# Kernel optimization log

Measured on AMD Instinct MI355X. Metric: run time of the kernel, lower is better.

Reference implementation:

```python
import jax, jax.numpy as jnp
import numpy as np

EMBED = 768
HEADS = 12
HEAD_DIM = EMBED // HEADS
B, T = 2, 2048


def setup_inputs() -> dict:
    key = jax.random.key(0)
    ks = jax.random.split(key, 5)
    scale = 0.02
    return {
        "x": jax.random.normal(ks[0], (B, T, EMBED), dtype=jnp.float32),
        "Wq": jax.random.normal(ks[1], (HEADS, EMBED, HEAD_DIM), dtype=jnp.float32) * scale,
        "Wk": jax.random.normal(ks[2], (HEADS, EMBED, HEAD_DIM), dtype=jnp.float32) * scale,
        "Wv": jax.random.normal(ks[3], (HEADS, EMBED, HEAD_DIM), dtype=jnp.float32) * scale,
        "Wp": jax.random.normal(ks[4], (EMBED, EMBED), dtype=jnp.float32) * scale,
        "bp": jnp.zeros((EMBED,), dtype=jnp.float32),
    }


def reference(x, Wq, Wk, Wv, Wp, bp):
    # x: [B,T,E]; per-head projections batched over the head axis.
    q = jnp.einsum("bte,hed->bhtd", x, Wq)  # [B,H,T,Dh]
    k = jnp.einsum("bte,hed->bhtd", x, Wk)
    v = jnp.einsum("bte,hed->bhtd", x, Wv)
    scale = 1.0 / jnp.sqrt(jnp.asarray(HEAD_DIM, dtype=x.dtype))
    scores = jnp.einsum("bhtd,bhsd->bhts", q, k) * scale  # [B,H,T,T]
    Tlen = x.shape[1]
    causal = jnp.tril(jnp.ones((Tlen, Tlen), dtype=bool))
    scores = jnp.where(causal[None, None], scores, jnp.asarray(-jnp.inf, dtype=scores.dtype))
    attn = jax.nn.softmax(scores, axis=-1)
    out = jnp.einsum("bhts,bhsd->bhtd", attn, v)  # [B,H,T,Dh]
    # concat heads (same layout as torch.cat over per-head outputs)
    out = out.transpose(0, 2, 1, 3).reshape(x.shape[0], Tlen, HEADS * HEAD_DIM)
    return out @ Wp + bp
```

## Files before the change

### kernel.cpp

```cpp
#include <hip/hip_runtime.h>
#include <math.h>

namespace {

constexpr int E_  = 768;
constexpr int H_  = 12;
constexpr int DH_ = 64;
constexpr int T_  = 2048;
constexpr int B_  = 2;
constexpr int M_  = B_ * T_;
constexpr int BH_ = B_ * H_;

typedef __attribute__((ext_vector_type(8))) short bf16x8;
typedef __attribute__((ext_vector_type(4))) float f32x4;

__device__ inline ushort f2bf(float f) {
  union { float f; unsigned u; } v; v.f = f;
  unsigned u = v.u + 0x7FFFu + ((v.u >> 16) & 1u);
  return (ushort)(u >> 16);
}
__device__ inline float bf2f(ushort u) {
  union { unsigned u; float f; } v; v.u = (unsigned)u << 16; return v.f;
}

__device__ __forceinline__ void gl16(const ushort* g, ushort* l) {
  __builtin_amdgcn_global_load_lds(
      (const __attribute__((address_space(1))) unsigned int*)(g),
      (__attribute__((address_space(3))) unsigned int*)(l), 16, 0, 0);
}

constexpr int NCONV = 1536;

__global__ __launch_bounds__(256) void prep_k(
    const float* __restrict__ x,
    const float* __restrict__ Wq, const float* __restrict__ Wk,
    const float* __restrict__ Wv, const float* __restrict__ Wp,
    ushort* __restrict__ xb, ushort* __restrict__ Wt, ushort* __restrict__ Wpt)
{
  __shared__ float tile[64][65];
  const int bid = blockIdx.x;
  const int tid = threadIdx.x;

  if (bid < NCONV) {
    const size_t i = ((size_t)bid * 256 + tid) * 8;
    float4 a = *(const float4*)(x + i);
    float4 b = *(const float4*)(x + i + 4);
    ushort o[8] = {f2bf(a.x), f2bf(a.y), f2bf(a.z), f2bf(a.w),
                   f2bf(b.x), f2bf(b.y), f2bf(b.z), f2bf(b.w)};
    *(bf16x8*)(xb + i) = *(bf16x8*)o;
    return;
  }

  const int wb = bid - NCONV;
  const int tr = tid >> 4, tc = tid & 15;
  const float* src; ushort* dst;
  int k0, n0, sN, dK;
  if (wb < 432) {
    const int mat = wb / 144, rem = wb % 144;
    const int h = rem / 12, ktile = rem % 12;
    const float* W = (mat == 0) ? Wq : (mat == 1) ? Wk : Wv;
    src = W + (size_t)h * E_ * DH_;
    dst = Wt + (size_t)(mat * H_ + h) * DH_ * E_;
    k0 = ktile * 64; n0 = 0; sN = DH_; dK = E_;
  } else {
    const int rem = wb - 432;
    src = Wp;
    dst = Wpt;
    k0 = (rem / 12) * 64; n0 = (rem % 12) * 64; sN = E_; dK = E_;
  }

#pragma unroll
  for (int rr = 0; rr < 64; rr += 16) {
    float4 v = *(const float4*)(src + (size_t)(k0 + tr + rr) * sN + n0 + tc * 4);
    tile[tr + rr][tc * 4 + 0] = v.x;
    tile[tr + rr][tc * 4 + 1] = v.y;
    tile[tr + rr][tc * 4 + 2] = v.z;
    tile[tr + rr][tc * 4 + 3] = v.w;
  }
  __syncthreads();
#pragma unroll
  for (int rr = 0; rr < 64; rr += 16) {
    const int n = tr + rr;
    ushort4 o;
    o.x = f2bf(tile[tc * 4 + 0][n]);
    o.y = f2bf(tile[tc * 4 + 1][n]);
    o.z = f2bf(tile[tc * 4 + 2][n]);
    o.w = f2bf(tile[tc * 4 + 3][n]);
    *(ushort4*)(dst + (size_t)(n0 + n) * dK + k0 + tc * 4) = o;
  }
}

constexpr float QSCALE = 0.18033688f;

__global__ __launch_bounds__(256) void qkv_fused_k(
    const ushort* __restrict__ xb, const ushort* __restrict__ Wt,
    ushort* __restrict__ q_ws, ushort* __restrict__ k_ws, ushort* __restrict__ vt_ws)
{
  __shared__ __align__(16) ushort lds[2 * 128 * 64];
  ushort* As = lds;
  ushort* Bs = lds + 128 * 64;

  const int n0 = blockIdx.x * 128;
  const int m0 = blockIdx.y * 128;

  const int tid  = threadIdx.x;
  const int w    = tid >> 6, l = tid & 63;
  const int lrow = l & 15, lk = l >> 4;
  const int r7   = lrow & 7;
  const int srow = l >> 3;
  const int sch  = (l & 7) ^ srow;

  f32x4 acc[2][8] = {};

  for (int k0 = 0; k0 < E_; k0 += 64) {
#pragma unroll
    for (int r = 0; r < 4; ++r) {
      const int base = r * 32 + w * 8;
      gl16(xb + (size_t)(m0 + base + srow) * E_ + k0 + sch * 8, &As[base * 64]);
      gl16(Wt + (size_t)(n0 + base + srow) * E_ + k0 + sch * 8, &Bs[base * 64]);
    }
    __syncthreads();

#pragma unroll
    for (int kk = 0; kk < 2; ++kk) {
      const int cof = ((kk * 4 + lk) ^ r7) * 8;
      const bf16x8 a0 = *(const bf16x8*)&As[(w * 32 + lrow) * 64 + cof];
      const bf16x8 a1 = *(const bf16x8*)&As[(w * 32 + 16 + lrow) * 64 + cof];
#pragma unroll
      for (int nf = 0; nf < 8; ++nf) {
        const bf16x8 b = *(const bf16x8*)&Bs[(nf * 16 + lrow) * 64 + cof];
        acc[0][nf] = __builtin_amdgcn_mfma_f32_16x16x32_bf16(a0, b, acc[0][nf], 0, 0, 0);
        acc[1][nf] = __builtin_amdgcn_mfma_f32_16x16x32_bf16(a1, b, acc[1][nf], 0, 0, 0);
      }
    }
    __syncthreads();
  }

  const int b  = m0 >> 11;
  const int t0 = m0 & 2047;
  ushort* Td = lds;

#pragma unroll
  for (int half = 0; half < 2; ++half) {
    const int seg = (n0 >> 6) + half;
    const int mat = seg / H_;
    const int h   = seg - mat * H_;
    const int bh  = b * H_ + h;

    if (mat != 2) {
      const float qs = (mat == 0) ? QSCALE : 1.0f;
      ushort* outw = (mat == 0) ? q_ws : k_ws;
#pragma unroll
      for (int mi = 0; mi < 2; ++mi)
#pragma unroll
        for (int i = 0; i < 4; ++i) {
          const int t = t0 + w * 32 + mi * 16 + lk * 4 + i;
          ushort* orow = outw + ((size_t)bh * T_ + t) * DH_;
#pragma unroll
          for (int nf2 = 0; nf2 < 4; ++nf2)
            orow[nf2 * 16 + lrow] = f2bf(acc[mi][half * 4 + nf2][i] * qs);
        }
    } else {
      __syncthreads();
#pragma unroll
      for (int mi = 0; mi < 2; ++mi)
#pragma unroll
        for (int i = 0; i < 4; ++i) {
          const int tl = w * 32 + mi * 16 + lk * 4 + i;
#pragma unroll
          for (int nf2 = 0; nf2 < 4; ++nf2)
            Td[(nf2 * 16 + lrow) * 136 + tl] = f2bf(acc[mi][half * 4 + nf2][i]);
        }
      __syncthreads();
#pragma unroll
      for (int it = 0; it < 4; ++it) {
        const int c = tid + it * 256;
        const int d = c >> 4, sub = c & 15;
        *(bf16x8*)(vt_ws + ((size_t)bh * DH_ + d) * T_ + t0 + sub * 8) =
            *(const bf16x8*)&Td[d * 136 + sub * 8];
      }
    }
  }
}

__global__ __launch_bounds__(256) void attn_split_k(
    const ushort* __restrict__ q_ws, const ushort* __restrict__ k_ws,
    const ushort* __restrict__ vt_ws, ushort* __restrict__ op_ws,
    float2* __restrict__ ml_ws)
{
  __shared__ __align__(16) ushort Ks[64 * 64];
  __shared__ __align__(16) ushort Vt[64 * 64];
  __shared__ __align__(16) ushort Pl[4][16 * 64];

  const int qt = 31 - (int)blockIdx.y;
  const int bh = blockIdx.x;
  const int hz = blockIdx.z;
  const int nt = qt + 1;
  const int klo = hz ? (nt >> 1) : 0;
  const int khi = hz ? nt : (nt >> 1);
  const int q0 = qt * 64;

  const ushort* Qb  = q_ws + (size_t)bh * T_ * DH_;
  const ushort* Kb  = k_ws + (size_t)bh * T_ * DH_;
  const ushort* VTb = vt_ws + (size_t)bh * DH_ * T_;

  const int tid  = threadIdx.x;
  const int w    = tid >> 6;
  const int l    = tid & 63;
  const int lrow = l & 15;
  const int lk   = l >> 4;
  const int r7   = lrow & 7;
  const int rr   = tid >> 3;
  const int sub  = tid & 7;
  const int swc  = sub ^ (rr & 7);

  const int st0 = rr * 64 + swc * 8;
  const int st1 = (rr + 32) * 64 + swc * 8;

  int kof0[4], kof1[4];
#pragma unroll
  for (int ct = 0; ct < 4; ++ct) {
    kof0[ct] = (ct * 16 + lrow) * 64 + ((lk ^ r7) * 8);
    kof1[ct] = (ct * 16 + lrow) * 64 + (((lk + 4) ^ r7) * 8);
  }

  const ushort* Qrow = Qb + (size_t)(q0 + w * 16 + lrow) * DH_;
  const bf16x8 qa0 = *(const bf16x8*)(Qrow + lk * 8);
  const bf16x8 qa1 = *(const bf16x8*)(Qrow + lk * 8 + 32);
  const int qglob = q0 + w * 16 + lrow;

  float m_r = -INFINITY, l_r = 0.f;
  f32x4 oc[4] = {};

  ushort* Pw = &Pl[w][0];
  const int rd0 = lrow * 64 + ((lk ^ r7) * 8);
  const int rd1 = lrow * 64 + (((lk + 4) ^ r7) * 8);
  const int wrbase  = lrow * 128 + (lk & 1) * 8;
  const int wrchunk = (lk >> 1);

  if (klo < khi) {
    bf16x8 kp0 = *(const bf16x8*)(Kb + (size_t)(klo * 64 + rr) * DH_ + sub * 8);
    bf16x8 kp1 = *(const bf16x8*)(Kb + (size_t)(klo * 64 + rr + 32) * DH_ + sub * 8);
    bf16x8 vp0 = *(const bf16x8*)(VTb + (size_t)rr * T_ + klo * 64 + sub * 8);
    bf16x8 vp1 = *(const bf16x8*)(VTb + (size_t)(rr + 32) * T_ + klo * 64 + sub * 8);

    for (int kt = klo; kt < khi; ++kt) {
      const int s0 = kt * 64;

      *(bf16x8*)&Ks[st0] = kp0;
      *(bf16x8*)&Ks[st1] = kp1;
      *(bf16x8*)&Vt[st0] = vp0;
      *(bf16x8*)&Vt[st1] = vp1;
      __syncthreads();

      if (kt + 1 < khi) {
        const int sn = s0 + 64;
        kp0 = *(const bf16x8*)(Kb + (size_t)(sn + rr) * DH_ + sub * 8);
        kp1 = *(const bf16x8*)(Kb + (size_t)(sn + rr + 32) * DH_ + sub * 8);
        vp0 = *(const bf16x8*)(VTb + (size_t)rr * T_ + sn + sub * 8);
        vp1 = *(const bf16x8*)(VTb + (size_t)(rr + 32) * T_ + sn + sub * 8);
      }

      f32x4 st[4];
#pragma unroll
      for (int ct = 0; ct < 4; ++ct) {
        const bf16x8 kb0 = *(const bf16x8*)&Ks[kof0[ct]];
        const bf16x8 kb1 = *(const bf16x8*)&Ks[kof1[ct]];
        f32x4 z = {0.f, 0.f, 0.f, 0.f};
        z = __builtin_amdgcn_mfma_f32_16x16x32_bf16(kb0, qa0, z, 0, 0, 0);
        st[ct] = __builtin_amdgcn_mfma_f32_16x16x32_bf16(kb1, qa1, z, 0, 0, 0);
      }

      if (kt == qt) {
#pragma unroll
        for (int ct = 0; ct < 4; ++ct)
#pragma unroll
          for (int i = 0; i < 4; ++i)
            if (s0 + ct * 16 + lk * 4 + i > qglob) st[ct][i] = -INFINITY;
      }

      float mc[4];
#pragma unroll
      for (int ct = 0; ct < 4; ++ct)
        mc[ct] = fmaxf(fmaxf(st[ct][0], st[ct][1]), fmaxf(st[ct][2], st[ct][3]));
      float mx = fmaxf(fmaxf(mc[0], mc[1]), fmaxf(mc[2], mc[3]));
      mx = fmaxf(mx, __shfl_xor(mx, 16));
      mx = fmaxf(mx, __shfl_xor(mx, 32));

      if (__any(mx > m_r + 8.f)) {
        const float mn   = fmaxf(m_r, mx);
        const float corr = exp2f(m_r - mn);
        m_r = mn;
        l_r *= corr;
#pragma unroll
        for (int i = 0; i < 4; ++i) {
          const float cr = __shfl(corr, lk * 4 + i);
#pragma unroll
          for (int ct = 0; ct < 4; ++ct) oc[ct][i] *= cr;
        }
      }

      float sc[4];
#pragma unroll
      for (int ct = 0; ct < 4; ++ct) {
#pragma unroll
        for (int i = 0; i < 4; ++i) st[ct][i] = exp2f(st[ct][i] - m_r);
        sc[ct] = (st[ct][0] + st[ct][1]) + (st[ct][2] + st[ct][3]);
      }
      float rs = (sc[0] + sc[1]) + (sc[2] + sc[3]);
      rs += __shfl_xor(rs, 16);
      rs += __shfl_xor(rs, 32);
      l_r += rs;

#pragma unroll
      for (int ct = 0; ct < 4; ++ct) {
        unsigned lo, hi;
        asm("v_cvt_pk_bf16_f32 %0, %1, %2" : "=v"(lo) : "v"(st[ct][0]), "v"(st[ct][1]));
        asm("v_cvt_pk_bf16_f32 %0, %1, %2" : "=v"(hi) : "v"(st[ct][2]), "v"(st[ct][3]));
        uint2 pk; pk.x = lo; pk.y = hi;
        const int ch = ((ct * 2 + wrchunk) ^ r7);
        *(uint2*)((char*)Pw + wrbase + ch * 16) = pk;
      }

      const bf16x8 pa0 = *(const bf16x8*)(Pw + rd0);
      const bf16x8 pa1 = *(const bf16x8*)(Pw + rd1);

#pragma unroll
      for (int ct = 0; ct < 4; ++ct) {
        const bf16x8 vb0 = *(const bf16x8*)&Vt[kof0[ct]];
        const bf16x8 vb1 = *(const bf16x8*)&Vt[kof1[ct]];
        oc[ct] = __builtin_amdgcn_mfma_f32_16x16x32_bf16(pa0, vb0, oc[ct], 0, 0, 0);
        oc[ct] = __builtin_amdgcn_mfma_f32_16x16x32_bf16(pa1, vb1, oc[ct], 0, 0, 0);
      }
      __syncthreads();
    }
  }

  const size_t pb = (size_t)(hz * BH_ + bh) * T_;
  if (lk == 0)
    ml_ws[pb + q0 + w * 16 + lrow] = make_float2(m_r, l_r);
#pragma unroll
  for (int i = 0; i < 4; ++i) {
    const int t = q0 + w * 16 + lk * 4 + i;
    ushort* orow = op_ws + (pb + t) * DH_;
#pragma unroll
    for (int ct = 0; ct < 4; ++ct)
      orow[ct * 16 + lrow] = f2bf(oc[ct][i]);
  }
}

__global__ __launch_bounds__(256) void attn_combine_k(
    const ushort* __restrict__ op_ws, const float2* __restrict__ ml_ws,
    ushort* __restrict__ o_ws)
{
  const int bh = blockIdx.x;
  const int t  = blockIdx.y * 64 + (threadIdx.x >> 2);
  const int d0 = (threadIdx.x & 3) * 16;

  const size_t ixA = (size_t)bh * T_ + t;
  const size_t ixB = (size_t)(BH_ + bh) * T_ + t;
  const float2 mlA = ml_ws[ixA];
  const float2 mlB = ml_ws[ixB];
  const float m   = fmaxf(mlA.x, mlB.x);
  const float wA  = exp2f(mlA.x - m);
  const float wB  = exp2f(mlB.x - m);
  const float inv = 1.0f / (wA * mlA.y + wB * mlB.y);

  const ushort* pA = op_ws + ixA * DH_ + d0;
  const ushort* pB = op_ws + ixB * DH_ + d0;
  bf16x8 a0 = *(const bf16x8*)pA;
  bf16x8 a1 = *(const bf16x8*)(pA + 8);
  bf16x8 b0 = *(const bf16x8*)pB;
  bf16x8 b1 = *(const bf16x8*)(pB + 8);

  ushort o[16];
#pragma unroll
  for (int j = 0; j < 8; ++j) {
    o[j]     = f2bf((wA * bf2f((ushort)a0[j]) + wB * bf2f((ushort)b0[j])) * inv);
    o[8 + j] = f2bf((wA * bf2f((ushort)a1[j]) + wB * bf2f((ushort)b1[j])) * inv);
  }
  const int bb = bh / H_, hh = bh - (bh / H_) * H_;
  ushort* po = o_ws + ((size_t)bb * T_ + t) * E_ + hh * DH_ + d0;
  *(bf16x8*)po       = *(const bf16x8*)&o[0];
  *(bf16x8*)(po + 8) = *(const bf16x8*)&o[8];
}

__global__ __launch_bounds__(256) void proj2_k(
    const ushort* __restrict__ ob, const ushort* __restrict__ Wpt,
    const float* __restrict__ bp, float* __restrict__ out)
{
  __shared__ __align__(16) ushort lds[2 * 128 * 64];
  ushort* As = lds;
  ushort* Bs = lds + 128 * 64;

  const int n0 = blockIdx.x * 128;
  const int m0 = blockIdx.y * 128;

  const int tid  = threadIdx.x;
  const int w    = tid >> 6, l = tid & 63;
  const int lrow = l & 15, lk = l >> 4;
  const int r7   = lrow & 7;
  const int srow = l >> 3;
  const int sch  = (l & 7) ^ srow;

  f32x4 acc[2][8] = {};

  for (int k0 = 0; k0 < E_; k0 += 64) {
#pragma unroll
    for (int r = 0; r < 4; ++r) {
      const int base = r * 32 + w * 8;
      gl16(ob  + (size_t)(m0 + base + srow) * E_ + k0 + sch * 8, &As[base * 64]);
      gl16(Wpt + (size_t)(n0 + base + srow) * E_ + k0 + sch * 8, &Bs[base * 64]);
    }
    __syncthreads();

#pragma unroll
    for (int kk = 0; kk < 2; ++kk) {
      const int cof = ((kk * 4 + lk) ^ r7) * 8;
      const bf16x8 a0 = *(const bf16x8*)&As[(w * 32 + lrow) * 64 + cof];
      const bf16x8 a1 = *(const bf16x8*)&As[(w * 32 + 16 + lrow) * 64 + cof];
#pragma unroll
      for (int nf = 0; nf < 8; ++nf) {
        const bf16x8 b = *(const bf16x8*)&Bs[(nf * 16 + lrow) * 64 + cof];
        acc[0][nf] = __builtin_amdgcn_mfma_f32_16x16x32_bf16(a0, b, acc[0][nf], 0, 0, 0);
        acc[1][nf] = __builtin_amdgcn_mfma_f32_16x16x32_bf16(a1, b, acc[1][nf], 0, 0, 0);
      }
    }
    __syncthreads();
  }

  float bias[8];
#pragma unroll
  for (int nf = 0; nf < 8; ++nf) bias[nf] = bp[n0 + nf * 16 + lrow];

#pragma unroll
  for (int mi = 0; mi < 2; ++mi)
#pragma unroll
    for (int i = 0; i < 4; ++i) {
      const int m = m0 + w * 32 + mi * 16 + lk * 4 + i;
      float* orow = out + (size_t)m * E_ + n0;
#pragma unroll
      for (int nf = 0; nf < 8; ++nf)
        orow[nf * 16 + lrow] = acc[mi][nf][i] + bias[nf];
    }
}

}

extern "C" void kernel_launch(void* const* d_in, const int* in_sizes, int n_in,
                              void* d_out, int out_size, void* d_ws, size_t ws_size,
                              hipStream_t stream) {
  const float* x  = (const float*)d_in[0];
  const float* Wq = (const float*)d_in[1];
  const float* Wk = (const float*)d_in[2];
  const float* Wv = (const float*)d_in[3];
  const float* Wp = (const float*)d_in[4];
  const float* bp = (const float*)d_in[5];
  float* out = (float*)d_out;

  const size_t nx  = (size_t)M_ * E_;
  const size_t nwt = (size_t)3 * H_ * DH_ * E_;
  const size_t nwp = (size_t)E_ * E_;
  const size_t per = (size_t)BH_ * T_ * DH_;

  ushort* xb    = (ushort*)d_ws;
  ushort* Wt    = xb + nx;
  ushort* Wpt   = Wt + nwt;
  ushort* q_ws  = Wpt + nwp;
  ushort* k_ws  = q_ws + per;
  ushort* vt_ws = k_ws + per;
  ushort* o_b   = vt_ws + per;
  ushort* op_ws = o_b + per;
  float2* ml_ws = (float2*)(op_ws + 2 * per);

  prep_k<<<dim3(NCONV + 576), 256, 0, stream>>>(x, Wq, Wk, Wv, Wp, xb, Wt, Wpt);
  qkv_fused_k<<<dim3(18, 32), 256, 0, stream>>>(xb, Wt, q_ws, k_ws, vt_ws);
  attn_split_k<<<dim3(24, 32, 2), 256, 0, stream>>>(q_ws, k_ws, vt_ws, op_ws, ml_ws);
  attn_combine_k<<<dim3(24, 32), 256, 0, stream>>>(op_ws, ml_ws, o_b);
  proj2_k<<<dim3(6, 32), 256, 0, stream>>>(o_b, Wpt, bp, out);
}
```

Before: 102.3 us.

## Fuse split-attention combine into projection GEMM and shrink QKV tile width

```diff
diff --git a/kernel.cpp b/kernel.cpp
--- a/kernel.cpp
+++ b/kernel.cpp
@@ -96,12 +96,14 @@
     const ushort* __restrict__ xb, const ushort* __restrict__ Wt,
     ushort* __restrict__ q_ws, ushort* __restrict__ k_ws, ushort* __restrict__ vt_ws)
 {
-  __shared__ __align__(16) ushort lds[2 * 128 * 64];
+  __shared__ __align__(16) ushort lds[(128 + 64) * 64];
   ushort* As = lds;
   ushort* Bs = lds + 128 * 64;
 
-  const int n0 = blockIdx.x * 128;
-  const int m0 = blockIdx.y * 128;
+  const int seg = blockIdx.x;
+  const int n0g = 0;
+  const int m0  = blockIdx.y * 128;
+  const ushort* Wh = Wt + (size_t)seg * DH_ * E_;
 
   const int tid  = threadIdx.x;
   const int w    = tid >> 6, l = tid & 63;
@@ -110,14 +112,15 @@
   const int srow = l >> 3;
   const int sch  = (l & 7) ^ srow;
 
-  f32x4 acc[2][8] = {};
+  f32x4 acc[2][4] = {};
 
   for (int k0 = 0; k0 < E_; k0 += 64) {
 #pragma unroll
     for (int r = 0; r < 4; ++r) {
       const int base = r * 32 + w * 8;
       gl16(xb + (size_t)(m0 + base + srow) * E_ + k0 + sch * 8, &As[base * 64]);
-      gl16(Wt + (size_t)(n0 + base + srow) * E_ + k0 + sch * 8, &Bs[base * 64]);
+      if (r < 2)
+        gl16(Wh + (size_t)(n0g + base + srow) * E_ + k0 + sch * 8, &Bs[base * 64]);
     }
     __syncthreads();
 
@@ -127,7 +130,7 @@
       const bf16x8 a0 = *(const bf16x8*)&As[(w * 32 + lrow) * 64 + cof];
       const bf16x8 a1 = *(const bf16x8*)&As[(w * 32 + 16 + lrow) * 64 + cof];
 #pragma unroll
-      for (int nf = 0; nf < 8; ++nf) {
+      for (int nf = 0; nf < 4; ++nf) {
         const bf16x8 b = *(const bf16x8*)&Bs[(nf * 16 + lrow) * 64 + cof];
         acc[0][nf] = __builtin_amdgcn_mfma_f32_16x16x32_bf16(a0, b, acc[0][nf], 0, 0, 0);
         acc[1][nf] = __builtin_amdgcn_mfma_f32_16x16x32_bf16(a1, b, acc[1][nf], 0, 0, 0);
@@ -136,49 +139,44 @@
     __syncthreads();
   }
 
-  const int b  = m0 >> 11;
-  const int t0 = m0 & 2047;
-  ushort* Td = lds;
-
-#pragma unroll
-  for (int half = 0; half < 2; ++half) {
-    const int seg = (n0 >> 6) + half;
-    const int mat = seg / H_;
-    const int h   = seg - mat * H_;
-    const int bh  = b * H_ + h;
-
-    if (mat != 2) {
-      const float qs = (mat == 0) ? QSCALE : 1.0f;
-      ushort* outw = (mat == 0) ? q_ws : k_ws;
-#pragma unroll
-      for (int mi = 0; mi < 2; ++mi)
-#pragma unroll
-        for (int i = 0; i < 4; ++i) {
-          const int t = t0 + w * 32 + mi * 16 + lk * 4 + i;
-          ushort* orow = outw + ((size_t)bh * T_ + t) * DH_;
-#pragma unroll
-          for (int nf2 = 0; nf2 < 4; ++nf2)
-            orow[nf2 * 16 + lrow] = f2bf(acc[mi][half * 4 + nf2][i] * qs);
-        }
-    } else {
-      __syncthreads();
-#pragma unroll
-      for (int mi = 0; mi < 2; ++mi)
-#pragma unroll
-        for (int i = 0; i < 4; ++i) {
-          const int tl = w * 32 + mi * 16 + lk * 4 + i;
-#pragma unroll
-          for (int nf2 = 0; nf2 < 4; ++nf2)
-            Td[(nf2 * 16 + lrow) * 136 + tl] = f2bf(acc[mi][half * 4 + nf2][i]);
-        }
-      __syncthreads();
-#pragma unroll
-      for (int it = 0; it < 4; ++it) {
-        const int c = tid + it * 256;
-        const int d = c >> 4, sub = c & 15;
-        *(bf16x8*)(vt_ws + ((size_t)bh * DH_ + d) * T_ + t0 + sub * 8) =
-            *(const bf16x8*)&Td[d * 136 + sub * 8];
-      }
+  const int b   = m0 >> 11;
+  const int t0  = m0 & 2047;
+  const int mat = seg / H_;
+  const int h   = seg - mat * H_;
+  const int bh  = b * H_ + h;
+
+  if (mat != 2) {
+    const float qs = (mat == 0) ? QSCALE : 1.0f;
+    ushort* outw = (mat == 0) ? q_ws : k_ws;
+#pragma unroll
+    for (int mi = 0; mi < 2; ++mi)
+#pragma unroll
+      for (int i = 0; i < 4; ++i) {
+        const int t = t0 + w * 32 + mi * 16 + lk * 4 + i;
+        ushort* orow = outw + ((size_t)bh * T_ + t) * DH_;
+#pragma unroll
+        for (int nf = 0; nf < 4; ++nf)
+          orow[nf * 16 + lrow] = f2bf(acc[mi][nf][i] * qs);
+      }
+  } else {
+    ushort* Td = lds;
+    __syncthreads();
+#pragma unroll
+    for (int mi = 0; mi < 2; ++mi)
+#pragma unroll
+      for (int i = 0; i < 4; ++i) {
+        const int tl = w * 32 + mi * 16 + lk * 4 + i;
+#pragma unroll
+        for (int nf = 0; nf < 4; ++nf)
+          Td[(nf * 16 + lrow) * 136 + tl] = f2bf(acc[mi][nf][i]);
+      }
+    __syncthreads();
+#pragma unroll
+    for (int it = 0; it < 4; ++it) {
+      const int c = tid + it * 256;
+      const int d = c >> 4, sub = c & 15;
+      *(bf16x8*)(vt_ws + ((size_t)bh * DH_ + d) * T_ + t0 + sub * 8) =
+          *(const bf16x8*)&Td[d * 136 + sub * 8];
     }
   }
 }
@@ -349,52 +347,19 @@
   }
 }
 
-__global__ __launch_bounds__(256) void attn_combine_k(
+__global__ __launch_bounds__(256) void proj_fused_k(
     const ushort* __restrict__ op_ws, const float2* __restrict__ ml_ws,
-    ushort* __restrict__ o_ws)
+    const ushort* __restrict__ Wpt, const float* __restrict__ bp,
+    float* __restrict__ out)
 {
-  const int bh = blockIdx.x;
-  const int t  = blockIdx.y * 64 + (threadIdx.x >> 2);
-  const int d0 = (threadIdx.x & 3) * 16;
-
-  const size_t ixA = (size_t)bh * T_ + t;
-  const size_t ixB = (size_t)(BH_ + bh) * T_ + t;
-  const float2 mlA = ml_ws[ixA];
-  const float2 mlB = ml_ws[ixB];
-  const float m   = fmaxf(mlA.x, mlB.x);
-  const float wA  = exp2f(mlA.x - m);
-  const float wB  = exp2f(mlB.x - m);
-  const float inv = 1.0f / (wA * mlA.y + wB * mlB.y);
-
-  const ushort* pA = op_ws + ixA * DH_ + d0;
-  const ushort* pB = op_ws + ixB * DH_ + d0;
-  bf16x8 a0 = *(const bf16x8*)pA;
-  bf16x8 a1 = *(const bf16x8*)(pA + 8);
-  bf16x8 b0 = *(const bf16x8*)pB;
-  bf16x8 b1 = *(const bf16x8*)(pB + 8);
-
-  ushort o[16];
-#pragma unroll
-  for (int j = 0; j < 8; ++j) {
-    o[j]     = f2bf((wA * bf2f((ushort)a0[j]) + wB * bf2f((ushort)b0[j])) * inv);
-    o[8 + j] = f2bf((wA * bf2f((ushort)a1[j]) + wB * bf2f((ushort)b1[j])) * inv);
-  }
-  const int bb = bh / H_, hh = bh - (bh / H_) * H_;
-  ushort* po = o_ws + ((size_t)bb * T_ + t) * E_ + hh * DH_ + d0;
-  *(bf16x8*)po       = *(const bf16x8*)&o[0];
-  *(bf16x8*)(po + 8) = *(const bf16x8*)&o[8];
-}
-
-__global__ __launch_bounds__(256) void proj2_k(
-    const ushort* __restrict__ ob, const ushort* __restrict__ Wpt,
-    const float* __restrict__ bp, float* __restrict__ out)
-{
-  __shared__ __align__(16) ushort lds[2 * 128 * 64];
+  __shared__ __align__(16) ushort lds[(64 + 64) * 64];
   ushort* As = lds;
-  ushort* Bs = lds + 128 * 64;
-
-  const int n0 = blockIdx.x * 128;
-  const int m0 = blockIdx.y * 128;
+  ushort* Bs = lds + 64 * 64;
+
+  const int n0 = blockIdx.x * 64;
+  const int m0 = blockIdx.y * 64;
+  const int b  = m0 >> 11;
+  const int t0 = m0 & 2047;
 
   const int tid  = threadIdx.x;
   const int w    = tid >> 6, l = tid & 63;
@@ -402,47 +367,76 @@
   const int r7   = lrow & 7;
   const int srow = l >> 3;
   const int sch  = (l & 7) ^ srow;
-
-  f32x4 acc[2][8] = {};
+  const int ar = tid >> 2;
+  const int cc = tid & 3;
+  const int a7 = ar & 7;
+
+  f32x4 acc[4] = {};
 
   for (int k0 = 0; k0 < E_; k0 += 64) {
-#pragma unroll
-    for (int r = 0; r < 4; ++r) {
+    const int h  = k0 >> 6;
+    const int bh = b * H_ + h;
+
+#pragma unroll
+    for (int r = 0; r < 2; ++r) {
       const int base = r * 32 + w * 8;
-      gl16(ob  + (size_t)(m0 + base + srow) * E_ + k0 + sch * 8, &As[base * 64]);
       gl16(Wpt + (size_t)(n0 + base + srow) * E_ + k0 + sch * 8, &Bs[base * 64]);
+    }
+
+    {
+      const int t = t0 + ar;
+      const size_t ixA = (size_t)bh * T_ + t;
+      const size_t ixB = (size_t)(BH_ + bh) * T_ + t;
+      const float2 mlA = ml_ws[ixA];
+      const float2 mlB = ml_ws[ixB];
+      const float m   = fmaxf(mlA.x, mlB.x);
+      const float wA  = exp2f(mlA.x - m);
+      const float wB  = exp2f(mlB.x - m);
+      const float inv = 1.0f / (wA * mlA.y + wB * mlB.y);
+      const float fA = wA * inv, fB = wB * inv;
+
+      const ushort* pA = op_ws + ixA * DH_ + cc * 16;
+      const ushort* pB = op_ws + ixB * DH_ + cc * 16;
+      bf16x8 a0 = *(const bf16x8*)pA;
+      bf16x8 a1 = *(const bf16x8*)(pA + 8);
+      bf16x8 b0 = *(const bf16x8*)pB;
+      bf16x8 b1 = *(const bf16x8*)(pB + 8);
+      ushort o[16];
+#pragma unroll
+      for (int j = 0; j < 8; ++j) {
+        o[j]     = f2bf(fA * bf2f((ushort)a0[j]) + fB * bf2f((ushort)b0[j]));
+        o[8 + j] = f2bf(fA * bf2f((ushort)a1[j]) + fB * bf2f((ushort)b1[j]));
+      }
+      *(bf16x8*)&As[ar * 64 + ((2 * cc) ^ a7) * 8]     = *(const bf16x8*)&o[0];
+      *(bf16x8*)&As[ar * 64 + ((2 * cc + 1) ^ a7) * 8] = *(const bf16x8*)&o[8];
     }
     __syncthreads();
 
 #pragma unroll
     for (int kk = 0; kk < 2; ++kk) {
       const int cof = ((kk * 4 + lk) ^ r7) * 8;
-      const bf16x8 a0 = *(const bf16x8*)&As[(w * 32 + lrow) * 64 + cof];
-      const bf16x8 a1 = *(const bf16x8*)&As[(w * 32 + 16 + lrow) * 64 + cof];
-#pragma unroll
-      for (int nf = 0; nf < 8; ++nf) {
-        const bf16x8 b = *(const bf16x8*)&Bs[(nf * 16 + lrow) * 64 + cof];
-        acc[0][nf] = __builtin_amdgcn_mfma_f32_16x16x32_bf16(a0, b, acc[0][nf], 0, 0, 0);
-        acc[1][nf] = __builtin_amdgcn_mfma_f32_16x16x32_bf16(a1, b, acc[1][nf], 0, 0, 0);
-      }
-    }
-    __syncthreads();
-  }
-
-  float bias[8];
-#pragma unroll
-  for (int nf = 0; nf < 8; ++nf) bias[nf] = bp[n0 + nf * 16 + lrow];
-
-#pragma unroll
-  for (int mi = 0; mi < 2; ++mi)
-#pragma unroll
-    for (int i = 0; i < 4; ++i) {
-      const int m = m0 + w * 32 + mi * 16 + lk * 4 + i;
-      float* orow = out + (size_t)m * E_ + n0;
-#pragma unroll
-      for (int nf = 0; nf < 8; ++nf)
-        orow[nf * 16 + lrow] = acc[mi][nf][i] + bias[nf];
-    }
+      const bf16x8 a = *(const bf16x8*)&As[(w * 16 + lrow) * 64 + cof];
+#pragma unroll
+      for (int nf = 0; nf < 4; ++nf) {
+        const bf16x8 bb = *(const bf16x8*)&Bs[(nf * 16 + lrow) * 64 + cof];
+        acc[nf] = __builtin_amdgcn_mfma_f32_16x16x32_bf16(a, bb, acc[nf], 0, 0, 0);
+      }
+    }
+    __syncthreads();
+  }
+
+  float bias[4];
+#pragma unroll
+  for (int nf = 0; nf < 4; ++nf) bias[nf] = bp[n0 + nf * 16 + lrow];
+
+#pragma unroll
+  for (int i = 0; i < 4; ++i) {
+    const int m = m0 + w * 16 + lk * 4 + i;
+    float* orow = out + (size_t)m * E_ + n0;
+#pragma unroll
+    for (int nf = 0; nf < 4; ++nf)
+      orow[nf * 16 + lrow] = acc[nf][i] + bias[nf];
+  }
 }
 
 }
@@ -469,13 +463,11 @@
   ushort* q_ws  = Wpt + nwp;
   ushort* k_ws  = q_ws + per;
   ushort* vt_ws = k_ws + per;
-  ushort* o_b   = vt_ws + per;
-  ushort* op_ws = o_b + per;
+  ushort* op_ws = vt_ws + per;
   float2* ml_ws = (float2*)(op_ws + 2 * per);
 
   prep_k<<<dim3(NCONV + 576), 256, 0, stream>>>(x, Wq, Wk, Wv, Wp, xb, Wt, Wpt);
-  qkv_fused_k<<<dim3(18, 32), 256, 0, stream>>>(xb, Wt, q_ws, k_ws, vt_ws);
+  qkv_fused_k<<<dim3(36, 32), 256, 0, stream>>>(xb, Wt, q_ws, k_ws, vt_ws);
   attn_split_k<<<dim3(24, 32, 2), 256, 0, stream>>>(q_ws, k_ws, vt_ws, op_ws, ml_ws);
-  attn_combine_k<<<dim3(24, 32), 256, 0, stream>>>(op_ws, ml_ws, o_b);
-  proj2_k<<<dim3(6, 32), 256, 0, stream>>>(o_b, Wpt, bp, out);
-}
+  proj_fused_k<<<dim3(12, 64), 256, 0, stream>>>(op_ws, ml_ws, Wpt, bp, out);
+}
```

Result: faster. 92.73 us (-9.3%).
